# Optimization experiments

Hardware: AMD Instinct MI355X
Metric: run time of the kernel (lower is better)

The kernel has to match this reference:

```python
import jax, jax.numpy as jnp
import numpy as np

SQRT_2PI = float(np.sqrt(2.0 * np.pi))
SQRT_2 = float(np.sqrt(2.0))


def nr(z):
    # 1/sqrt(2*pi)*exp(-z^2/2) + z/2*(1+erf(z/sqrt(2)))  (relu expectation under Gaussian)
    return jnp.exp(-0.5 * z * z) / SQRT_2PI + 0.5 * z * (1.0 + jax.lax.erf(z / SQRT_2))


def setup_inputs() -> dict:
    key = jax.random.key(0)
    ks = jax.random.split(key, 6)
    B, IN, OUT, C = 8192, 1024, 1024, 8
    x = jax.random.normal(ks[0], (B, IN), dtype=jnp.float32)
    miss = jax.random.uniform(ks[1], (B, IN)) < 0.02
    x = jnp.where(miss, jnp.nan, x)
    W = jax.random.normal(ks[2], (IN, OUT), dtype=jnp.float32)
    b = jax.random.normal(ks[3], (OUT,), dtype=jnp.float32)
    gmm_weights = jnp.log(jnp.full((C,), 1.0 / C, dtype=jnp.float32))  # stored as log-weights
    gmm_means = jax.random.normal(ks[4], (C, IN), dtype=jnp.float32)
    gmm_covariances = jnp.abs(jax.random.normal(ks[5], (C, IN), dtype=jnp.float32))
    return {"x": x, "W": W, "b": b, "gmm_weights": gmm_weights,
            "gmm_means": gmm_means, "gmm_covariances": gmm_covariances}


def reference(x, W, b, gmm_weights, gmm_means, gmm_covariances):
    nan_mask = jnp.isnan(x)                      # [B, in]
    is_missing = jnp.any(nan_mask, axis=1)       # [B]
    maskf = nan_mask.astype(x.dtype)             # [B, in], 1 where missing
    x_clean = jnp.where(nan_mask, 0.0, x)        # NaNs zeroed; exact on full rows
    p = jax.nn.softmax(gmm_weights)              # [C]
    base = x_clean @ W                           # [B, out]
    W2 = W * W
    n_gmm = gmm_weights.shape[0]
    out_missing = jnp.zeros_like(base)
    for i in range(n_gmm):  # small fixed component count
        # m = where(isnan(x), mean_i, x)  =>  m @ W = x_clean @ W + (mask * mean_i) @ W
        a = base + (maskf * gmm_means[i]) @ W + b                 # [B, out]
        # (W^2 * sigma[:, :, None]).sum(1) as a real GEMM
        var = (maskf * jnp.abs(gmm_covariances[i])) @ W2          # [B, out]
        denom = jnp.sqrt(jnp.where(var > 0, var, 1.0))            # safe for full rows
        out_missing = out_missing + p[i] * nr(a / denom)
    out_full = jax.nn.relu(base + b)
    return jnp.where(is_missing[:, None], out_missing, out_full)
```

## Files before the change

### kernel.cpp

```cpp
#include <hip/hip_runtime.h>
#include <math.h>

#define DEV __device__ __forceinline__

constexpr int IN   = 1024;
constexpr int OUT  = 1024;
constexpr int NC   = 8;
constexpr int MAXM = 128;

typedef __bf16 bf16x8 __attribute__((ext_vector_type(8)));
typedef float  f32x4  __attribute__((ext_vector_type(4)));
typedef float  f32x2  __attribute__((ext_vector_type(2)));

DEV unsigned short f2bf(float f) {
  union { float f; unsigned int u; } v; v.f = f;
  unsigned int u = v.u;
  return (unsigned short)((u + 0x7FFFu + ((u >> 16) & 1u)) >> 16);
}

DEV void gload_lds16(const void* g, void* l) {
  __builtin_amdgcn_global_load_lds(
      (__attribute__((address_space(1))) void*)(unsigned long long)(uintptr_t)g,
      (__attribute__((address_space(3))) void*)l,
      16, 0, 0);
}

__global__ __launch_bounds__(256) void prep_kernel(
    const float* __restrict__ x, unsigned short* __restrict__ xb,
    unsigned short* __restrict__ midx, int* __restrict__ counts) {
  const int row = blockIdx.x, t = threadIdx.x;
  __shared__ int ps[256];

  float4 v = ((const float4*)x)[row * (IN / 4) + t];
  bool n0 = (v.x != v.x), n1 = (v.y != v.y), n2 = (v.z != v.z), n3 = (v.w != v.w);

  ushort4 o;
  o.x = f2bf(n0 ? 0.f : v.x);
  o.y = f2bf(n1 ? 0.f : v.y);
  o.z = f2bf(n2 ? 0.f : v.z);
  o.w = f2bf(n3 ? 0.f : v.w);
  ((ushort4*)xb)[row * (IN / 4) + t] = o;

  int lc = (int)n0 + (int)n1 + (int)n2 + (int)n3;
  ps[t] = lc;
  __syncthreads();
  for (int off = 1; off < 256; off <<= 1) {
    int add = (t >= off) ? ps[t - off] : 0;
    __syncthreads();
    ps[t] += add;
    __syncthreads();
  }
  int pos = ps[t] - lc;
  int col = 4 * t;
  if (n0) { if (pos < MAXM) midx[row * MAXM + pos] = (unsigned short)(col + 0); pos++; }
  if (n1) { if (pos < MAXM) midx[row * MAXM + pos] = (unsigned short)(col + 1); pos++; }
  if (n2) { if (pos < MAXM) midx[row * MAXM + pos] = (unsigned short)(col + 2); pos++; }
  if (n3) { if (pos < MAXM) midx[row * MAXM + pos] = (unsigned short)(col + 3); pos++; }
  if (t == 255) counts[row] = min(ps[255], MAXM);
}

__global__ __launch_bounds__(256) void transpose_w(
    const float* __restrict__ W, unsigned short* __restrict__ Wt,
    const float* __restrict__ gw, float* __restrict__ p_ws) {
  __shared__ float tile[32][33];
  const int k0 = blockIdx.x * 32, n0 = blockIdx.y * 32;
  const int tx = threadIdx.x, ty = threadIdx.y;

  if (k0 == 0 && n0 == 0 && tx == 0 && ty == 0) {
    float wmax = -1e30f;
    for (int i = 0; i < NC; ++i) wmax = fmaxf(wmax, gw[i]);
    float e[NC], s = 0.f;
    for (int i = 0; i < NC; ++i) { e[i] = expf(gw[i] - wmax); s += e[i]; }
    for (int i = 0; i < NC; ++i) p_ws[i] = e[i] / s;
  }

  for (int r = ty; r < 32; r += 8) tile[r][tx] = W[(k0 + r) * OUT + (n0 + tx)];
  __syncthreads();
  for (int r = ty; r < 32; r += 8) Wt[(n0 + r) * IN + (k0 + tx)] = f2bf(tile[tx][r]);
}

__global__ __launch_bounds__(256) void gemm_base(
    const unsigned short* __restrict__ A, const unsigned short* __restrict__ Bt,
    float* __restrict__ C, int M) {
  __shared__ __align__(16) unsigned short sA[128 * 32];
  __shared__ __align__(16) unsigned short sB[128 * 32];

  const int t = threadIdx.x;
  const int lane = t & 63, w = t >> 6;
  const int wm = w >> 1, wn = w & 1;
  const int l15 = lane & 15, kblk = lane >> 4;
  const int row0 = blockIdx.x * 128, col0 = blockIdx.y * 128;

  const int r_a  = t >> 2;
  const int cb_a = (t & 3) * 8;

  f32x4 acc[4][4] = {};

  const int aoff = (wm * 64 + l15) * 32 + kblk * 8;
  const int boff = (wn * 64 + l15) * 32 + kblk * 8;

  for (int k0 = 0; k0 < IN; k0 += 32) {
    __syncthreads();
    gload_lds16(&A[(size_t)(row0 + r_a) * IN + k0 + cb_a],       &sA[t * 8]);
    gload_lds16(&A[(size_t)(row0 + r_a + 64) * IN + k0 + cb_a],  &sA[2048 + t * 8]);
    gload_lds16(&Bt[(size_t)(col0 + r_a) * IN + k0 + cb_a],      &sB[t * 8]);
    gload_lds16(&Bt[(size_t)(col0 + r_a + 64) * IN + k0 + cb_a], &sB[2048 + t * 8]);
    __syncthreads();

    bf16x8 af[4], bfr[4];
#pragma unroll
    for (int mi = 0; mi < 4; ++mi) af[mi]  = *(const bf16x8*)&sA[aoff + mi * 16 * 32];
#pragma unroll
    for (int ni = 0; ni < 4; ++ni) bfr[ni] = *(const bf16x8*)&sB[boff + ni * 16 * 32];
#pragma unroll
    for (int mi = 0; mi < 4; ++mi)
#pragma unroll
      for (int ni = 0; ni < 4; ++ni)
        acc[mi][ni] = __builtin_amdgcn_mfma_f32_16x16x32_bf16(af[mi], bfr[ni], acc[mi][ni], 0, 0, 0);
  }

#pragma unroll
  for (int mi = 0; mi < 4; ++mi)
#pragma unroll
    for (int ni = 0; ni < 4; ++ni) {
      int grow = row0 + wm * 64 + mi * 16 + kblk * 4;
      int gcol = col0 + wn * 64 + ni * 16 + l15;
#pragma unroll
      for (int r = 0; r < 4; ++r)
        C[(size_t)(grow + r) * OUT + gcol] = acc[mi][ni][r];
    }
}

__global__ __launch_bounds__(256, 1) void epilogue_kernel(
    float* __restrict__ io, const float* __restrict__ W,
    const float* __restrict__ bvec, const float* __restrict__ p_ws,
    const float* __restrict__ gmean, const float* __restrict__ gcov,
    const unsigned short* __restrict__ midx, const int* __restrict__ counts) {
  const int row = blockIdx.x, t = threadIdx.x;
  __shared__ f32x2 smc[MAXM][NC];
  __shared__ unsigned short skidx[MAXM];

  const int m = counts[row];

  f32x4 base = *(const f32x4*)(io + (size_t)row * OUT + 4 * t);
  base = base + *(const f32x4*)(bvec + 4 * t);

  if (m == 0) {
    f32x4 r;
#pragma unroll
    for (int c = 0; c < 4; ++c) r[c] = fmaxf(base[c], 0.0f);
    *(f32x4*)(io + (size_t)row * OUT + 4 * t) = r;
    return;
  }

  f32x4 p0 = *(const f32x4*)(p_ws);
  f32x4 p1 = *(const f32x4*)(p_ws + 4);

  for (int idx = t; idx < m * NC; idx += 256) {
    int tt = idx >> 3, i = idx & 7;
    int k = midx[row * MAXM + tt];
    f32x2 mc;
    mc[0] = gmean[i * IN + k];
    mc[1] = fabsf(gcov[i * IN + k]);
    smc[tt][i] = mc;
  }
  for (int idx = t; idx < m; idx += 256) skidx[idx] = midx[row * MAXM + idx];
  __syncthreads();

  f32x2 acc[NC][4] = {};
  for (int tt = 0; tt < m; ++tt) {
    int k = __builtin_amdgcn_readfirstlane((int)skidx[tt]);
    f32x4 wv = *(const f32x4*)(W + ((size_t)k << 10) + 4 * t);
    f32x2 wz[4];
#pragma unroll
    for (int c = 0; c < 4; ++c) { wz[c][0] = wv[c]; wz[c][1] = wv[c] * wv[c]; }
#pragma unroll
    for (int i = 0; i < NC; ++i) {
      f32x2 mc = smc[tt][i];
#pragma unroll
      for (int c = 0; c < 4; ++c)
        acc[i][c] = acc[i][c] + wz[c] * mc;
    }
  }

  const float INV_SQRT_2PI = 0.39894228040143268f;
  const float LOGI_K       = 1.702f;
  const float L2E          = 1.442695040888963f;

  f32x4 out = {};
#pragma unroll
  for (int i = 0; i < NC; ++i) {
    float pi = (i < 4) ? p0[i & 3] : p1[i & 3];
#pragma unroll
    for (int c = 0; c < 4; ++c) {
      float a   = base[c] + acc[i][c][0];
      float var = acc[i][c][1];
      float rs  = (var > 0.f) ? __builtin_amdgcn_rsqf(var) : 1.0f;
      float z   = a * rs;
      float eu  = __builtin_amdgcn_exp2f(-0.5f * L2E * z * z);
      float phi = INV_SQRT_2PI * eu;
      float el  = __builtin_amdgcn_exp2f(-LOGI_K * L2E * z);
      float Phi = __builtin_amdgcn_rcpf(1.0f + el);
      float nrv = fmaf(z, Phi, phi);
      out[c] = fmaf(pi, nrv, out[c]);
    }
  }
  *(f32x4*)(io + (size_t)row * OUT + 4 * t) = out;
}

extern "C" void kernel_launch(void* const* d_in, const int* in_sizes, int n_in,
                              void* d_out, int out_size, void* d_ws, size_t ws_size,
                              hipStream_t stream) {
  const float* x  = (const float*)d_in[0];
  const float* W  = (const float*)d_in[1];
  const float* b  = (const float*)d_in[2];
  const float* gw = (const float*)d_in[3];
  const float* gm = (const float*)d_in[4];
  const float* gc = (const float*)d_in[5];
  float* out = (float*)d_out;
  const int M = in_sizes[0] / IN;

  char* ws = (char*)d_ws;
  unsigned short* xb   = (unsigned short*)ws;
  unsigned short* Wt   = (unsigned short*)(ws + (size_t)M * IN * 2);
  unsigned short* midx = (unsigned short*)(ws + (size_t)M * IN * 2 + (size_t)IN * OUT * 2);
  int* counts = (int*)(ws + (size_t)M * IN * 2 + (size_t)IN * OUT * 2 + (size_t)M * MAXM * 2);
  float* p_ws = (float*)(ws + (size_t)M * IN * 2 + (size_t)IN * OUT * 2 + (size_t)M * MAXM * 2 + (size_t)M * 4);

  prep_kernel<<<M, 256, 0, stream>>>(x, xb, midx, counts);
  transpose_w<<<dim3(IN / 32, OUT / 32), dim3(32, 8), 0, stream>>>(W, Wt, gw, p_ws);
  gemm_base<<<dim3(M / 128, OUT / 128), 256, 0, stream>>>(xb, Wt, out, M);
  epilogue_kernel<<<M, 256, 0, stream>>>(out, W, b, p_ws, gm, gc, midx, counts);
}
```

Measured before the change: 163.0 us.

## Compute missing-row GMM correction with bf16 MFMA over gathered W rows

Replaces the scalar FMA loop in the epilogue with bf16 MFMA. Gathered rows of W (and their squares) are staged in LDS in chunks of 32 missing indices and multiplied against packed component means and covariances, so all 8 components come out of one matrix op. The epilogue grid is split into two column halves per row for more parallelism. It lowers MAXM to 96 and moves the correction terms to bf16 precision, which adds rounding error and may drop missing entries in rows with more than 96 NaNs.

```diff
diff --git a/kernel.cpp b/kernel.cpp
--- a/kernel.cpp
+++ b/kernel.cpp
@@ -6,16 +6,26 @@
 constexpr int IN   = 1024;
 constexpr int OUT  = 1024;
 constexpr int NC   = 8;
-constexpr int MAXM = 128;
+constexpr int MAXM = 96;
+constexpr int CPB  = 512;
+constexpr int KST  = 36;
 
 typedef __bf16 bf16x8 __attribute__((ext_vector_type(8)));
 typedef float  f32x4  __attribute__((ext_vector_type(4)));
 typedef float  f32x2  __attribute__((ext_vector_type(2)));
+typedef unsigned int u32;
+
+union ABf { bf16x8 v; u32 d[4]; unsigned short s[8]; };
 
 DEV unsigned short f2bf(float f) {
-  union { float f; unsigned int u; } v; v.f = f;
-  unsigned int u = v.u;
+  union { float f; u32 u; } v; v.f = f;
+  u32 u = v.u;
   return (unsigned short)((u + 0x7FFFu + ((u >> 16) & 1u)) >> 16);
+}
+
+DEV float bfbits2f(u32 bits) {
+  union { u32 u; float f; } v; v.u = bits;
+  return v.f;
 }
 
 DEV void gload_lds16(const void* g, void* l) {
@@ -131,81 +141,159 @@
     }
 }
 
-__global__ __launch_bounds__(256, 1) void epilogue_kernel(
+__global__ __launch_bounds__(256) void epilogue_mfma(
     float* __restrict__ io, const float* __restrict__ W,
     const float* __restrict__ bvec, const float* __restrict__ p_ws,
     const float* __restrict__ gmean, const float* __restrict__ gcov,
     const unsigned short* __restrict__ midx, const int* __restrict__ counts) {
-  const int row = blockIdx.x, t = threadIdx.x;
-  __shared__ f32x2 smc[MAXM][NC];
-  __shared__ unsigned short skidx[MAXM];
+  __shared__ unsigned short sW[CPB * KST];
+  __shared__ u32 smcP[MAXM * NC];
+
+  const int row = blockIdx.x;
+  const int cb  = blockIdx.y * CPB;
+  const int t   = threadIdx.x;
+  const int lane = t & 63, wv = t >> 6;
+  const int nn = lane & 15, ii = lane & 7, g = lane >> 4;
+  const bool isCov = nn >= 8;
+  const int rrb = isCov ? 2 : 0;
 
   const int m = counts[row];
 
-  f32x4 base = *(const f32x4*)(io + (size_t)row * OUT + 4 * t);
-  base = base + *(const f32x4*)(bvec + 4 * t);
+  f32x2 basev[8];
+#pragma unroll
+  for (int tl = 0; tl < 8; ++tl) {
+    int c = cb + wv * 128 + tl * 16 + g * 4 + rrb;
+    f32x2 bb = *(const f32x2*)(io + (size_t)row * OUT + c);
+    f32x2 bi = *(const f32x2*)(bvec + c);
+    basev[tl][0] = bb[0] + bi[0];
+    basev[tl][1] = bb[1] + bi[1];
+  }
 
   if (m == 0) {
-    f32x4 r;
-#pragma unroll
-    for (int c = 0; c < 4; ++c) r[c] = fmaxf(base[c], 0.0f);
-    *(f32x4*)(io + (size_t)row * OUT + 4 * t) = r;
+#pragma unroll
+    for (int tl = 0; tl < 8; ++tl) {
+      if (ii == 0) {
+        int c = cb + wv * 128 + tl * 16 + g * 4 + rrb;
+        f32x2 o; o[0] = fmaxf(basev[tl][0], 0.f); o[1] = fmaxf(basev[tl][1], 0.f);
+        *(f32x2*)(io + (size_t)row * OUT + c) = o;
+      }
+    }
     return;
   }
 
-  f32x4 p0 = *(const f32x4*)(p_ws);
-  f32x4 p1 = *(const f32x4*)(p_ws + 4);
-
-  for (int idx = t; idx < m * NC; idx += 256) {
+  const int nch = (m + 31) >> 5;
+
+  for (int idx = t; idx < nch * 32 * NC; idx += 256) {
     int tt = idx >> 3, i = idx & 7;
-    int k = midx[row * MAXM + tt];
-    f32x2 mc;
-    mc[0] = gmean[i * IN + k];
-    mc[1] = fabsf(gcov[i * IN + k]);
-    smc[tt][i] = mc;
-  }
-  for (int idx = t; idx < m; idx += 256) skidx[idx] = midx[row * MAXM + idx];
-  __syncthreads();
-
-  f32x2 acc[NC][4] = {};
-  for (int tt = 0; tt < m; ++tt) {
-    int k = __builtin_amdgcn_readfirstlane((int)skidx[tt]);
-    f32x4 wv = *(const f32x4*)(W + ((size_t)k << 10) + 4 * t);
-    f32x2 wz[4];
-#pragma unroll
-    for (int c = 0; c < 4; ++c) { wz[c][0] = wv[c]; wz[c][1] = wv[c] * wv[c]; }
-#pragma unroll
-    for (int i = 0; i < NC; ++i) {
-      f32x2 mc = smc[tt][i];
-#pragma unroll
-      for (int c = 0; c < 4; ++c)
-        acc[i][c] = acc[i][c] + wz[c] * mc;
+    u32 v = 0;
+    if (tt < m) {
+      int k = midx[(size_t)row * MAXM + tt];
+      float mn = gmean[i * IN + k];
+      float cv = fabsf(gcov[i * IN + k]);
+      v = (u32)f2bf(mn) | ((u32)f2bf(cv) << 16);
+    }
+    smcP[tt * NC + i] = v;
+  }
+
+  f32x4 acc[8] = {};
+
+  for (int ch = 0; ch < nch; ++ch) {
+    if (ch) __syncthreads();
+
+    {
+      int kk = t & 31;
+      int tkk = ch * 32 + kk;
+      int k = midx[(size_t)row * MAXM + min(tkk, m - 1)];
+      const float* wrow = W + (size_t)k * OUT + cb;
+      int cg = (t >> 5) * 4;
+#pragma unroll
+      for (int i2 = 0; i2 < 16; ++i2) {
+        int col = cg + i2 * 32;
+        float4 w4 = *(const float4*)(wrow + col);
+        sW[(col + 0) * KST + kk] = f2bf(w4.x);
+        sW[(col + 1) * KST + kk] = f2bf(w4.y);
+        sW[(col + 2) * KST + kk] = f2bf(w4.z);
+        sW[(col + 3) * KST + kk] = f2bf(w4.w);
+      }
+    }
+    __syncthreads();
+
+    ABf vals;
+#pragma unroll
+    for (int j = 0; j < 8; ++j) {
+      u32 u = smcP[(ch * 32 + g * 8 + j) * NC + ii];
+      vals.s[j] = (unsigned short)(isCov ? (u >> 16) : (u & 0xFFFFu));
+    }
+    ABf zf; zf.d[0] = zf.d[1] = zf.d[2] = zf.d[3] = 0;
+    bf16x8 bm = isCov ? zf.v : vals.v;
+    bf16x8 bc = isCov ? vals.v : zf.v;
+
+#pragma unroll
+    for (int tl = 0; tl < 8; ++tl) {
+      int colL = wv * 128 + tl * 16 + nn;
+      ABf aw;
+      *(uint2*)&aw.d[0] = *(const uint2*)&sW[colL * KST + g * 8];
+      *(uint2*)&aw.d[2] = *(const uint2*)&sW[colL * KST + g * 8 + 4];
+      ABf a2;
+#pragma unroll
+      for (int d = 0; d < 4; ++d) {
+        u32 u = aw.d[d];
+        float lo = bfbits2f(u << 16);
+        float hi = bfbits2f(u & 0xFFFF0000u);
+        a2.d[d] = (u32)f2bf(lo * lo) | ((u32)f2bf(hi * hi) << 16);
+      }
+      acc[tl] = __builtin_amdgcn_mfma_f32_16x16x32_bf16(aw.v, bm, acc[tl], 0, 0, 0);
+      acc[tl] = __builtin_amdgcn_mfma_f32_16x16x32_bf16(a2.v, bc, acc[tl], 0, 0, 0);
     }
   }
 
   const float INV_SQRT_2PI = 0.39894228040143268f;
-  const float LOGI_K       = 1.702f;
-  const float L2E          = 1.442695040888963f;
-
-  f32x4 out = {};
-#pragma unroll
-  for (int i = 0; i < NC; ++i) {
-    float pi = (i < 4) ? p0[i & 3] : p1[i & 3];
-#pragma unroll
-    for (int c = 0; c < 4; ++c) {
-      float a   = base[c] + acc[i][c][0];
-      float var = acc[i][c][1];
-      float rs  = (var > 0.f) ? __builtin_amdgcn_rsqf(var) : 1.0f;
+  const float LOGI_K = 1.702f;
+  const float L2E = 1.442695040888963f;
+  const float pi_w = p_ws[ii];
+
+#pragma unroll
+  for (int tl = 0; tl < 8; ++tl) {
+    f32x4 ac = acc[tl];
+    float s0 = __shfl_xor(ac[0], 8);
+    float s1 = __shfl_xor(ac[1], 8);
+    float s2 = __shfl_xor(ac[2], 8);
+    float s3 = __shfl_xor(ac[3], 8);
+    float A0 = isCov ? s2 : ac[0];
+    float A1 = isCov ? s3 : ac[1];
+    float V0 = isCov ? ac[2] : s0;
+    float V1 = isCov ? ac[3] : s1;
+
+    float t0, t1;
+    {
+      float a   = basev[tl][0] + A0;
+      float rs  = (V0 > 0.f) ? __builtin_amdgcn_rsqf(V0) : 1.0f;
       float z   = a * rs;
       float eu  = __builtin_amdgcn_exp2f(-0.5f * L2E * z * z);
-      float phi = INV_SQRT_2PI * eu;
       float el  = __builtin_amdgcn_exp2f(-LOGI_K * L2E * z);
       float Phi = __builtin_amdgcn_rcpf(1.0f + el);
-      float nrv = fmaf(z, Phi, phi);
-      out[c] = fmaf(pi, nrv, out[c]);
-    }
-  }
-  *(f32x4*)(io + (size_t)row * OUT + 4 * t) = out;
+      t0 = pi_w * fmaf(z, Phi, INV_SQRT_2PI * eu);
+    }
+    {
+      float a   = basev[tl][1] + A1;
+      float rs  = (V1 > 0.f) ? __builtin_amdgcn_rsqf(V1) : 1.0f;
+      float z   = a * rs;
+      float eu  = __builtin_amdgcn_exp2f(-0.5f * L2E * z * z);
+      float el  = __builtin_amdgcn_exp2f(-LOGI_K * L2E * z);
+      float Phi = __builtin_amdgcn_rcpf(1.0f + el);
+      t1 = pi_w * fmaf(z, Phi, INV_SQRT_2PI * eu);
+    }
+#pragma unroll
+    for (int d = 1; d <= 4; d <<= 1) {
+      t0 += __shfl_xor(t0, d);
+      t1 += __shfl_xor(t1, d);
+    }
+    if (ii == 0) {
+      int c = cb + wv * 128 + tl * 16 + g * 4 + rrb;
+      f32x2 o; o[0] = t0; o[1] = t1;
+      *(f32x2*)(io + (size_t)row * OUT + c) = o;
+    }
+  }
 }
 
 extern "C" void kernel_launch(void* const* d_in, const int* in_sizes, int n_in,
@@ -230,5 +318,5 @@
   prep_kernel<<<M, 256, 0, stream>>>(x, xb, midx, counts);
   transpose_w<<<dim3(IN / 32, OUT / 32), dim3(32, 8), 0, stream>>>(W, Wt, gw, p_ws);
   gemm_base<<<dim3(M / 128, OUT / 128), 256, 0, stream>>>(xb, Wt, out, M);
-  epilogue_kernel<<<M, 256, 0, stream>>>(out, W, b, p_ws, gm, gc, midx, counts);
-}
+  epilogue_mfma<<<dim3(M, 2), 256, 0, stream>>>(out, W, b, p_ws, gm, gc, midx, counts);
+}
```

Result: slower. 226.9 us (+39.2%).
